# Kernel tuning notes

Measured on AMD Instinct MI355X. Metric: run time of the kernel, lower is better.

## Reference

```python
import jax, jax.numpy as jnp
import numpy as np

K_NB = 16
HID = 64
CIN = 128
EPS = 1e-5


def knn_idx(q, t, k):
    # q [B,N,3] queries, t [B,M,3] targets -> idx [B,N,k] into targets
    d = (jnp.sum(q * q, -1)[:, :, None] + jnp.sum(t * t, -1)[:, None, :]
         - 2.0 * jnp.einsum('bnd,bmd->bnm', q, t))
    _, idx = jax.lax.top_k(-d, k)
    return idx


def gather(feat, idx):
    # feat [B,C,M], idx [B,N,K] -> [B,C,N,K]
    return jax.vmap(lambda f, i: f[:, i])(feat, idx)


def conv1x1(x, W, b):
    # x [B,C,N,K], W [O,C], b [O]
    return jnp.einsum('oc,bcnk->bonk', W, x) + b[None, :, None, None]


def group_norm(x, gamma, beta, groups):
    B, C, N, K = x.shape
    xg = x.reshape(B, groups, C // groups, N, K)
    m = xg.mean(axis=(2, 3, 4), keepdims=True)
    v = xg.var(axis=(2, 3, 4), keepdims=True)
    xg = (xg - m) / jnp.sqrt(v + EPS)
    x = xg.reshape(B, C, N, K)
    return x * gamma[None, :, None, None] + beta[None, :, None, None]


def leaky(x):
    return jnp.where(x >= 0, x, 0.1 * x)


def setup_inputs() -> dict:
    key = jax.random.key(0)
    ks = jax.random.split(key, 20)
    B, N = 2, 4096
    d = {
        'xyz0': jax.random.normal(ks[0], (B, 3, N), jnp.float32),
        'xyz1': jax.random.normal(ks[1], (B, 3, N), jnp.float32),
        'state': jax.random.normal(ks[2], (B, HID, N), jnp.float32),
        'corr0': jax.random.normal(ks[3], (B, HID, N), jnp.float32),
        'feat0': jax.random.normal(ks[4], (B, CIN, N), jnp.float32),
        'feat1': jax.random.normal(ks[5], (B, CIN, N), jnp.float32),
        'flow0': jax.random.normal(ks[6], (B, 3, N), jnp.float32),
        # flow_layer: SetConv(3, [64,64]) -> convs take 3+3=6 then 64 in-chans
        'fw1': jax.random.normal(ks[7], (64, 6), jnp.float32) * 0.05,
        'fb1': jnp.zeros((64,), jnp.float32),
        'fg1': jnp.ones((64,), jnp.float32),
        'fbe1': jnp.zeros((64,), jnp.float32),
        'fw2': jax.random.normal(ks[8], (64, 64), jnp.float32) * 0.05,
        'fb2': jnp.zeros((64,), jnp.float32),
        'fg2': jnp.ones((64,), jnp.float32),
        'fbe2': jnp.zeros((64,), jnp.float32),
        # GRU gates: SetConv in_feat = hid(64)+(hid+64=128)=192, +3 = 195 -> 64, no act
        'wz': jax.random.normal(ks[9], (HID, 195), jnp.float32) * 0.05,
        'bz': jnp.zeros((HID,), jnp.float32),
        'wr': jax.random.normal(ks[10], (HID, 195), jnp.float32) * 0.05,
        'br': jnp.zeros((HID,), jnp.float32),
        'wq': jax.random.normal(ks[11], (HID, 195), jnp.float32) * 0.05,
        'bq': jnp.zeros((HID,), jnp.float32),
        # interp weight_net: 2*128+3=259 -> 128 -> 64
        'wa1': jax.random.normal(ks[12], (CIN, 2 * CIN + 3), jnp.float32) * 0.05,
        'ba1': jnp.zeros((CIN,), jnp.float32),
        'wa2': jax.random.normal(ks[13], (HID, CIN), jnp.float32) * 0.05,
        'ba2': jnp.zeros((HID,), jnp.float32),
    }
    return d


def reference(xyz0, xyz1, state, corr0, feat0, feat1, flow0,
              fw1, fb1, fg1, fbe1, fw2, fb2, fg2, fbe2,
              wz, bz, wr, br, wq, bq, wa1, ba1, wa2, ba2):
    xyz0_t = xyz0.transpose(0, 2, 1)  # [B,N,3]
    xyz1_t = xyz1.transpose(0, 2, 1)

    # ---- flow_layer: SetConv (KNN, N==npoint so new_xyz = xyz0) ----
    idx0 = knn_idx(xyz0_t, xyz0_t, K_NB)              # [B,N,K]
    gxyz0 = gather(xyz0, idx0) - xyz0[:, :, :, None]  # [B,3,N,K]
    h = jnp.concatenate([gather(flow0, idx0), gxyz0], axis=1)  # [B,6,N,K]
    h = leaky(group_norm(conv1x1(h, fw1, fb1), fg1, fbe1, 64 // 16))
    h = leaky(group_norm(conv1x1(h, fw2, fb2), fg2, fbe2, 64 // 16))
    flow_feat = h.max(axis=3)  # [B,64,N]

    # ---- iter_layer: SetGRU over xyz0 neighbors ----
    feat_g = jnp.concatenate([corr0, flow_feat], axis=1)  # [B,128,N]

    def gate(f, W, b):
        g = jnp.concatenate([gather(f, idx0), gxyz0], axis=1)
        return conv1x1(g, W, b).max(axis=3)  # [B,64,N]

    hid_in = jnp.concatenate([feat_g, state], axis=1)  # [B,192,N]
    z = jax.nn.sigmoid(gate(hid_in, wz, bz))
    r = jax.nn.sigmoid(gate(hid_in, wr, br))
    q = jnp.tanh(gate(jnp.concatenate([feat_g, r * state], axis=1), wq, bq))
    next_state = (1.0 - z) * state + z * q  # [B,64,N]

    # ---- align_layer: SetInterp (queries xyz1, targets xyz0) ----
    idx1 = knn_idx(xyz1_t, xyz0_t, K_NB)
    gv = gather(next_state, idx1)                        # [B,64,N,K]
    gx = gather(xyz0, idx1) - xyz1[:, :, :, None]        # [B,3,N,K]
    gf = jnp.concatenate([
        gather(feat0, idx1),
        jnp.broadcast_to(feat1[:, :, :, None], feat1.shape + (K_NB,))], axis=1)
    w = conv1x1(jnp.concatenate([gf, gx], axis=1), wa1, ba1)
    w = conv1x1(leaky(w), wa2, ba2)
    w = jax.nn.softmax(w, axis=3)
    return jnp.sum(gv * w, axis=3)  # [B,64,N]
```

## Files before the change

kernel.cpp:

```cpp
#include <hip/hip_runtime.h>

#define B_SZ 2

__device__ __forceinline__ int rfl(int x) { return __builtin_amdgcn_readfirstlane(x); }
__device__ __forceinline__ float leaky(float v) { return v >= 0.f ? v : 0.1f * v; }

__launch_bounds__(256)
__global__ void pack_kernel(const float* __restrict__ xyz, float4* __restrict__ out, int N)
{
  int b = blockIdx.y;
  int i = blockIdx.x * 256 + threadIdx.x;
  if (i >= N) return;
  const float* p = xyz + (size_t)b * 3 * N;
  float x = p[i], y = p[N + i], z = p[2 * N + i];
  out[(size_t)b * N + i] = make_float4(x, y, z, x * x + y * y + z * z);
}

__launch_bounds__(256)
__global__ void knn_wave_kernel(const float4* __restrict__ pk,
    const float* __restrict__ q0, const float* __restrict__ q1,
    int* __restrict__ idx0, int* __restrict__ idx1, int N, int PN)
{
  __shared__ __align__(16) float4 ts[1024];
  __shared__ uint2 buf[4][256];
  const int lane = threadIdx.x & 63, wav = rfl(threadIdx.x >> 6);
  const int qg = blockIdx.x * 4 + wav;
  const bool src1 = qg >= PN;
  const int qloc = src1 ? qg - PN : qg;
  const int b = qloc / N;
  const int n = qloc - b * N;
  const float* qb = (src1 ? q1 : q0) + (size_t)b * 3 * N;
  const float qx = qb[n], qy = qb[N + n], qz = qb[2 * N + n];
  const float qq = qx * qx + qy * qy + qz * qz;
  const float4* pb = pk + (size_t)b * N;

  float lmin = 3.0e38f;
  for (int ch = 0; ch < N; ch += 1024) {
    __syncthreads();
    for (int i = threadIdx.x; i < 1024; i += 256) ts[i] = pb[ch + i];
    __syncthreads();
#pragma unroll 4
    for (int sub = 0; sub < 16; ++sub) {
      float4 v = ts[sub * 64 + lane];
      float key = (qq + v.w) - 2.0f * (qx * v.x + qy * v.y + qz * v.z);
      lmin = fminf(lmin, key);
    }
  }
  float gm = fminf(lmin, __shfl_xor(lmin, 1, 64));
  gm = fminf(gm, __shfl_xor(gm, 2, 64));
  float t0 = gm;
  t0 = fmaxf(t0, __shfl_xor(t0, 4, 64));
  t0 = fmaxf(t0, __shfl_xor(t0, 8, 64));
  t0 = fmaxf(t0, __shfl_xor(t0, 16, 64));
  t0 = fmaxf(t0, __shfl_xor(t0, 32, 64));

  int cnt = 0;
  for (int ch = 0; ch < N; ch += 1024) {
    __syncthreads();
    for (int i = threadIdx.x; i < 1024; i += 256) ts[i] = pb[ch + i];
    __syncthreads();
    for (int sub = 0; sub < 16; ++sub) {
      float4 v = ts[sub * 64 + lane];
      float key = (qq + v.w) - 2.0f * (qx * v.x + qy * v.y + qz * v.z);
      bool qf = key <= t0;
      unsigned long long mask = __ballot(qf);
      if (mask) {
        unsigned lo = __builtin_amdgcn_mbcnt_lo((unsigned)mask, 0u);
        unsigned pre = __builtin_amdgcn_mbcnt_hi((unsigned)(mask >> 32), lo);
        if (qf) {
          unsigned slot = (unsigned)cnt + pre;
          if (slot < 256u)
            buf[wav][slot] = make_uint2(__float_as_uint(key),
                                        (unsigned)(ch + sub * 64 + lane));
        }
        cnt += (int)__popcll(mask);
      }
    }
  }
  int C = cnt < 256 ? cnt : 256;
  int* op = src1 ? idx1 : idx0;
  size_t base = ((size_t)b * N + n) * 16;

  if (C <= 64) {
    float kd = 3.0e38f; int ki = 0x7fffffff;
    if (lane < C) { uint2 u = buf[wav][lane]; kd = __uint_as_float(u.x); ki = (int)u.y; }
    int rank = 0;
    for (int j = 0; j < C; ++j) {
      uint2 u = buf[wav][j];
      float kj = __uint_as_float(u.x); int ij = (int)u.y;
      rank += ((kj < kd) || (kj == kd && ij < ki)) ? 1 : 0;
    }
    if (lane < C && rank < 16) op[base + rank] = ki;
  } else {
    float kd[4]; int ki[4]; int rank[4] = {0, 0, 0, 0};
#pragma unroll
    for (int e = 0; e < 4; ++e) {
      int j = e * 64 + lane;
      if (j < C) { uint2 u = buf[wav][j]; kd[e] = __uint_as_float(u.x); ki[e] = (int)u.y; }
      else { kd[e] = 3.0e38f; ki[e] = 0x7fffffff; }
    }
    for (int j = 0; j < C; ++j) {
      uint2 u = buf[wav][j];
      float kj = __uint_as_float(u.x); int ij = (int)u.y;
#pragma unroll
      for (int e = 0; e < 4; ++e)
        rank[e] += ((kj < kd[e]) || (kj == kd[e] && ij < ki[e])) ? 1 : 0;
    }
#pragma unroll
    for (int e = 0; e < 4; ++e)
      if (e * 64 + lane < C && rank[e] < 16) op[base + rank[e]] = ki[e];
  }
}

__launch_bounds__(256)
__global__ void prep_w_kernel(const float* __restrict__ wz, const float* __restrict__ wr,
    const float* __restrict__ wq, const float* __restrict__ wa1, const float* __restrict__ wa2,
    const float* __restrict__ bz, const float* __restrict__ br,
    float* __restrict__ WtZR, float* __restrict__ WtQ,
    float* __restrict__ WtU, float* __restrict__ WtV, float* __restrict__ WtA2,
    float* __restrict__ bZR)
{
  int job = blockIdx.x;
  int tid = threadIdx.x;
  if (job == 0) {
    for (int e = tid; e < 195 * 128; e += 256) {
      int k = e >> 7, o = e & 127;
      const float* w = (o < 64) ? wz : wr;
      WtZR[(size_t)k * 128 + o] = w[(size_t)(o & 63) * 195 + k];
    }
    if (tid < 128) bZR[tid] = (tid < 64) ? bz[tid] : br[tid - 64];
  } else if (job == 1) {
    for (int e = tid; e < 195 * 64; e += 256) {
      int k = e >> 6, o = e & 63;
      WtQ[(size_t)k * 64 + o] = wq[(size_t)o * 195 + k];
    }
  } else if (job == 2) {
    for (int e = tid; e < 131 * 128; e += 256) {
      int k = e >> 7, o = e & 127;
      int col = (k < 128) ? k : 256 + (k - 128);
      WtU[(size_t)k * 128 + o] = wa1[(size_t)o * 259 + col];
    }
  } else if (job == 3) {
    for (int e = tid; e < 131 * 128; e += 256) {
      int k = e >> 7, o = e & 127;
      float v = (k < 128) ? wa1[(size_t)o * 259 + 128 + k]
                          : -wa1[(size_t)o * 259 + 256 + (k - 128)];
      WtV[(size_t)k * 128 + o] = v;
    }
  } else {
    for (int e = tid; e < 128 * 64; e += 256) {
      int c = e >> 6, o = e & 63;
      WtA2[e] = wa2[(size_t)o * 128 + c];
    }
  }
}

#define KC 66
__launch_bounds__(256)
__global__ void projT_kernel(const float* __restrict__ Wt, int K, int WOUT,
    const float* __restrict__ bias, float* __restrict__ out,
    int N, int PN,
    const float* __restrict__ s0, int c0, int l0,
    const float* __restrict__ s1, int c1, int l1,
    const float* __restrict__ s2, int c2, int l2,
    const float* __restrict__ s3, int c3, int l3)
{
  __shared__ __align__(16) float Ws[KC][68];
  __shared__ __align__(16) float Xs[KC][68];
  const int n0 = blockIdx.x * 64;
  const int oo = blockIdx.y * 64;
  const int b = n0 / N;
  const int nn0 = n0 - b * N;
  const int tid = threadIdx.x;
  const int tx = tid & 15, ty = tid >> 4;
  const int o4 = tx * 4, n4 = ty * 4;
  float acc[4][4];
#pragma unroll
  for (int i = 0; i < 4; ++i)
#pragma unroll
    for (int j = 0; j < 4; ++j)
      acc[i][j] = bias ? bias[oo + o4 + j] : 0.0f;

  const int e01 = c0 + c1, e012 = c0 + c1 + c2;
  for (int k0 = 0; k0 < K; k0 += KC) {
    const int kc = min(KC, K - k0);
    __syncthreads();
    for (int e = tid; e < kc * 64; e += 256) {
      int k = e >> 6, o = e & 63;
      Ws[k][o] = Wt[(size_t)(k0 + k) * WOUT + oo + o];
    }
    for (int e = tid; e < kc * 64; e += 256) {
      int k = e >> 6, j = e & 63;
      int c = k0 + k;
      float v;
      if (c < c0)        v = l0 ? s0[(size_t)c * PN + n0 + j]
                                : s0[((size_t)b * c0 + c) * N + nn0 + j];
      else if (c < e01)  { int cc = c - c0;
                           v = l1 ? s1[(size_t)cc * PN + n0 + j]
                                  : s1[((size_t)b * c1 + cc) * N + nn0 + j]; }
      else if (c < e012) { int cc = c - e01;
                           v = l2 ? s2[(size_t)cc * PN + n0 + j]
                                  : s2[((size_t)b * c2 + cc) * N + nn0 + j]; }
      else               { int cc = c - e012;
                           v = l3 ? s3[(size_t)cc * PN + n0 + j]
                                  : s3[((size_t)b * c3 + cc) * N + nn0 + j]; }
      Xs[k][j] = v;
    }
    __syncthreads();
#pragma unroll 2
    for (int k = 0; k < kc; ++k) {
      float4 wv = *(const float4*)&Ws[k][o4];
      float4 xv = *(const float4*)&Xs[k][n4];
      acc[0][0] = fmaf(xv.x, wv.x, acc[0][0]); acc[0][1] = fmaf(xv.x, wv.y, acc[0][1]);
      acc[0][2] = fmaf(xv.x, wv.z, acc[0][2]); acc[0][3] = fmaf(xv.x, wv.w, acc[0][3]);
      acc[1][0] = fmaf(xv.y, wv.x, acc[1][0]); acc[1][1] = fmaf(xv.y, wv.y, acc[1][1]);
      acc[1][2] = fmaf(xv.y, wv.z, acc[1][2]); acc[1][3] = fmaf(xv.y, wv.w, acc[1][3]);
      acc[2][0] = fmaf(xv.z, wv.x, acc[2][0]); acc[2][1] = fmaf(xv.z, wv.y, acc[2][1]);
      acc[2][2] = fmaf(xv.z, wv.z, acc[2][2]); acc[2][3] = fmaf(xv.z, wv.w, acc[2][3]);
      acc[3][0] = fmaf(xv.w, wv.x, acc[3][0]); acc[3][1] = fmaf(xv.w, wv.y, acc[3][1]);
      acc[3][2] = fmaf(xv.w, wv.z, acc[3][2]); acc[3][3] = fmaf(xv.w, wv.w, acc[3][3]);
    }
  }
#pragma unroll
  for (int i = 0; i < 4; ++i) {
    float4 r = make_float4(acc[i][0], acc[i][1], acc[i][2], acc[i][3]);
    *(float4*)&out[(size_t)(n0 + n4 + i) * WOUT + oo + o4] = r;
  }
}

__launch_bounds__(256)
__global__ void projUV_kernel(const float* __restrict__ WtU, const float* __restrict__ WtV,
    const float* __restrict__ ba1, float* __restrict__ Uo, float* __restrict__ Vo,
    int N, int PN,
    const float* __restrict__ feat0, const float* __restrict__ feat1,
    const float* __restrict__ x0, const float* __restrict__ x1)
{
  __shared__ __align__(16) float Ws[KC][68];
  __shared__ __align__(16) float Xs[KC][68];
  const int z = blockIdx.z;
  const float* Wt = z ? WtV : WtU;
  const float* bias = z ? ba1 : 0;
  float* out = z ? Vo : Uo;
  const float* s0 = z ? feat1 : feat0;
  const float* s1 = z ? x1 : x0;
  const int K = 131, WOUT = 128, c0 = 128;
  const int n0 = blockIdx.x * 64;
  const int oo = blockIdx.y * 64;
  const int b = n0 / N;
  const int nn0 = n0 - b * N;
  const int tid = threadIdx.x;
  const int tx = tid & 15, ty = tid >> 4;
  const int o4 = tx * 4, n4 = ty * 4;
  float acc[4][4];
#pragma unroll
  for (int i = 0; i < 4; ++i)
#pragma unroll
    for (int j = 0; j < 4; ++j)
      acc[i][j] = bias ? bias[oo + o4 + j] : 0.0f;

  for (int k0 = 0; k0 < K; k0 += KC) {
    const int kc = min(KC, K - k0);
    __syncthreads();
    for (int e = tid; e < kc * 64; e += 256) {
      int k = e >> 6, o = e & 63;
      Ws[k][o] = Wt[(size_t)(k0 + k) * WOUT + oo + o];
    }
    for (int e = tid; e < kc * 64; e += 256) {
      int k = e >> 6, j = e & 63;
      int c = k0 + k;
      float v;
      if (c < c0) v = s0[((size_t)b * c0 + c) * N + nn0 + j];
      else        v = s1[((size_t)b * 3 + (c - c0)) * N + nn0 + j];
      Xs[k][j] = v;
    }
    __syncthreads();
#pragma unroll 2
    for (int k = 0; k < kc; ++k) {
      float4 wv = *(const float4*)&Ws[k][o4];
      float4 xv = *(const float4*)&Xs[k][n4];
      acc[0][0] = fmaf(xv.x, wv.x, acc[0][0]); acc[0][1] = fmaf(xv.x, wv.y, acc[0][1]);
      acc[0][2] = fmaf(xv.x, wv.z, acc[0][2]); acc[0][3] = fmaf(xv.x, wv.w, acc[0][3]);
      acc[1][0] = fmaf(xv.y, wv.x, acc[1][0]); acc[1][1] = fmaf(xv.y, wv.y, acc[1][1]);
      acc[1][2] = fmaf(xv.y, wv.z, acc[1][2]); acc[1][3] = fmaf(xv.y, wv.w, acc[1][3]);
      acc[2][0] = fmaf(xv.z, wv.x, acc[2][0]); acc[2][1] = fmaf(xv.z, wv.y, acc[2][1]);
      acc[2][2] = fmaf(xv.z, wv.z, acc[2][2]); acc[2][3] = fmaf(xv.z, wv.w, acc[2][3]);
      acc[3][0] = fmaf(xv.w, wv.x, acc[3][0]); acc[3][1] = fmaf(xv.w, wv.y, acc[3][1]);
      acc[3][2] = fmaf(xv.w, wv.z, acc[3][2]); acc[3][3] = fmaf(xv.w, wv.w, acc[3][3]);
    }
  }
#pragma unroll
  for (int i = 0; i < 4; ++i) {
    float4 r = make_float4(acc[i][0], acc[i][1], acc[i][2], acc[i][3]);
    *(float4*)&out[(size_t)(n0 + n4 + i) * WOUT + oo + o4] = r;
  }
}

__device__ __forceinline__ void seg_accumL(const float* __restrict__ p, int cnt,
    const float* __restrict__ WL, int sC, int sN, long n0, float acc[4])
{
#pragma unroll 4
  for (int c = 0; c < cnt; ++c) {
    float w = WL[c];
    const float* pp = p + (size_t)c * sC + (size_t)n0 * sN;
#pragma unroll
    for (int m = 0; m < 4; ++m)
      acc[m] = fmaf(w, pp[(size_t)m * sN], acc[m]);
  }
}

template<int WP>
__launch_bounds__(256)
__global__ void proj_kernel(
    const float* __restrict__ W0, const float* __restrict__ bias,
    float* __restrict__ out, int OUTS, int wld, int N,
    const float* __restrict__ s0, int c0, int w0,
    const float* __restrict__ s1, int c1, int w1)
{
  __shared__ float Wl[64 * WP];
  const int b = blockIdx.y;
  const int lane = threadIdx.x & 63;
  const int wav = rfl(threadIdx.x >> 6);
  for (int r = wav; r < 64; r += 4)
    for (int c = lane; c < c0; c += 64)
      Wl[r * WP + c] = W0[(size_t)r * wld + w0 + c];
  for (int r = wav; r < 64; r += 4)
    for (int c = lane; c < c1; c += 64)
      Wl[r * WP + c0 + c] = W0[(size_t)r * wld + w1 + c];
  __syncthreads();
  const long n0 = ((long)blockIdx.x * 4 + wav) * 4;
  float bv = bias ? bias[lane] : 0.0f;
  float acc[4] = {bv, bv, bv, bv};
  const float* WL = &Wl[lane * WP];
  seg_accumL(s0 + (size_t)b * c0 * N, c0, WL, N, 1, n0, acc);
  seg_accumL(s1 + (size_t)b * c1 * N, c1, WL + c0, N, 1, n0, acc);
#pragma unroll
  for (int m = 0; m < 4; ++m)
    out[((size_t)b * N + n0 + m) * OUTS + lane] = acc[m];
}

__launch_bounds__(256)
__global__ void gn1_stats_kernel(const float* __restrict__ G1, const float* __restrict__ xyz0,
    const float* __restrict__ fw1, const int* __restrict__ idx0,
    float* __restrict__ stats1, int N)
{
  __shared__ float red[4][4][2];
  int b = blockIdx.y;
  int lane = threadIdx.x & 63, wav = rfl(threadIdx.x >> 6);
  float wg0 = fw1[lane * 6 + 3], wg1 = fw1[lane * 6 + 4], wg2 = fw1[lane * 6 + 5];
  const float* xb = xyz0 + (size_t)b * 3 * N;
  float sum = 0.f, sq = 0.f;
  for (int n = blockIdx.x * 4 + wav; n < N; n += gridDim.x * 4) {
    const int* ip = idx0 + ((size_t)b * N + n) * 16;
    float bx = wg0 * xb[n] + wg1 * xb[N + n] + wg2 * xb[2 * N + n];
#pragma unroll
    for (int k = 0; k < 16; ++k) {
      int m = ip[k];
      float y = G1[((size_t)b * N + m) * 64 + lane] - bx;
      sum += y; sq += y * y;
    }
  }
#pragma unroll
  for (int off = 1; off < 16; off <<= 1) {
    sum += __shfl_xor(sum, off, 64);
    sq += __shfl_xor(sq, off, 64);
  }
  int g = lane >> 4;
  if ((lane & 15) == 0) { red[wav][g][0] = sum; red[wav][g][1] = sq; }
  __syncthreads();
  if (threadIdx.x < 8) {
    int gg = threadIdx.x >> 1, s = threadIdx.x & 1;
    float v = red[0][gg][s] + red[1][gg][s] + red[2][gg][s] + red[3][gg][s];
    atomicAdd(&stats1[(b * 4 + gg) * 2 + s], v);
  }
}

__launch_bounds__(256, 2)
__global__ void conv2_kernel(const float* __restrict__ G1, const float* __restrict__ xyz0,
    const float* __restrict__ fw1, const int* __restrict__ idx0,
    const float* __restrict__ fw2, const float* __restrict__ fb2,
    const float* __restrict__ fg1, const float* __restrict__ fbe1,
    const float* __restrict__ raw1, float cnt,
    float* __restrict__ y2max, float* __restrict__ y2min,
    float* __restrict__ stats2, int N)
{
  __shared__ __align__(16) float x2[4][16][64];
  __shared__ float red[4][4][2];
  const int b = blockIdx.y;
  const int lane = threadIdx.x & 63;
  const int wav = rfl(threadIdx.x >> 6);
  float4 w[16];
#pragma unroll
  for (int i = 0; i < 16; ++i) w[i] = *(const float4*)&fw2[lane * 64 + i * 4];
  float wg0 = fw1[lane * 6 + 3], wg1 = fw1[lane * 6 + 4], wg2 = fw1[lane * 6 + 5];
  const int g = lane >> 4;
  float s_ = raw1[(b * 4 + g) * 2], q_ = raw1[(b * 4 + g) * 2 + 1];
  float mu1 = s_ / cnt;
  float inv1 = rsqrtf(q_ / cnt - mu1 * mu1 + 1e-5f);
  float sc1 = fg1[lane] * inv1;
  float sh1 = fbe1[lane] - mu1 * sc1;
  float fb2l = fb2[lane];
  const float* xb = xyz0 + (size_t)b * 3 * N;
  float sum = 0.f, sq = 0.f;
  for (int n = blockIdx.x * 4 + wav; n < N; n += gridDim.x * 4) {
    const int* ip = idx0 + ((size_t)b * N + n) * 16;
    float bx = wg0 * xb[n] + wg1 * xb[N + n] + wg2 * xb[2 * N + n];
#pragma unroll
    for (int k = 0; k < 16; ++k) {
      int m = ip[k];
      float y = G1[((size_t)b * N + m) * 64 + lane] - bx;
      x2[wav][k][lane] = leaky(y * sc1 + sh1);
    }
    float acc[16];
#pragma unroll
    for (int k = 0; k < 16; ++k) acc[k] = fb2l;
#pragma unroll
    for (int c4 = 0; c4 < 16; ++c4) {
      float4 w4 = w[c4];
#pragma unroll
      for (int k = 0; k < 16; ++k) {
        float4 x4 = *(const float4*)&x2[wav][k][c4 * 4];
        acc[k] = fmaf(w4.x, x4.x, acc[k]);
        acc[k] = fmaf(w4.y, x4.y, acc[k]);
        acc[k] = fmaf(w4.z, x4.z, acc[k]);
        acc[k] = fmaf(w4.w, x4.w, acc[k]);
      }
    }
    float mx = -3.0e38f, mn = 3.0e38f;
#pragma unroll
    for (int k = 0; k < 16; ++k) {
      mx = fmaxf(mx, acc[k]); mn = fminf(mn, acc[k]);
      sum += acc[k]; sq += acc[k] * acc[k];
    }
    y2max[((size_t)b * N + n) * 64 + lane] = mx;
    y2min[((size_t)b * N + n) * 64 + lane] = mn;
  }
#pragma unroll
  for (int off = 1; off < 16; off <<= 1) {
    sum += __shfl_xor(sum, off, 64);
    sq += __shfl_xor(sq, off, 64);
  }
  if ((lane & 15) == 0) { red[wav][g][0] = sum; red[wav][g][1] = sq; }
  __syncthreads();
  if (threadIdx.x < 8) {
    int gg = threadIdx.x >> 1, s = threadIdx.x & 1;
    float v = red[0][gg][s] + red[1][gg][s] + red[2][gg][s] + red[3][gg][s];
    atomicAdd(&stats2[(b * 4 + gg) * 2 + s], v);
  }
}

__launch_bounds__(256)
__global__ void flow_feat_kernel(const float* __restrict__ y2max, const float* __restrict__ y2min,
    const float* __restrict__ raw2, float cnt,
    const float* __restrict__ fg2, const float* __restrict__ fbe2,
    float* __restrict__ ff_t, int N, int PN)
{
  size_t i = (size_t)blockIdx.x * blockDim.x + threadIdx.x;
  if (i >= (size_t)B_SZ * N * 64) return;
  int c = i & 63;
  size_t pn = i >> 6;
  int b = (int)(pn / N);
  int g = c >> 4;
  float s_ = raw2[(b * 4 + g) * 2], q_ = raw2[(b * 4 + g) * 2 + 1];
  float mu = s_ / cnt;
  float inv = rsqrtf(q_ / cnt - mu * mu + 1e-5f);
  float sc = fg2[c] * inv;
  float sh = fbe2[c] - mu * sc;
  float y = (sc >= 0.0f) ? y2max[i] : y2min[i];
  ff_t[(size_t)c * PN + pn] = leaky(y * sc + sh);
}

__launch_bounds__(256)
__global__ void gate_zr_kernel(const float* __restrict__ Szr,
    const float* __restrict__ wz, const float* __restrict__ wr,
    const float* __restrict__ xyz0, const float* __restrict__ state,
    const int* __restrict__ idx0,
    float* __restrict__ zo, float* __restrict__ rs_t, int N, int PN)
{
  int b = blockIdx.y;
  int lane = threadIdx.x & 63, wav = rfl(threadIdx.x >> 6);
  float wz0 = wz[lane * 195 + 192], wz1 = wz[lane * 195 + 193], wz2 = wz[lane * 195 + 194];
  float wr0 = wr[lane * 195 + 192], wr1 = wr[lane * 195 + 193], wr2 = wr[lane * 195 + 194];
  const float* xb = xyz0 + (size_t)b * 3 * N;
  for (int n = blockIdx.x * 4 + wav; n < N; n += gridDim.x * 4) {
    const int* ip = idx0 + ((size_t)b * N + n) * 16;
    float u0 = xb[n], u1 = xb[N + n], u2 = xb[2 * N + n];
    float xz = wz0 * u0 + wz1 * u1 + wz2 * u2;
    float xr = wr0 * u0 + wr1 * u1 + wr2 * u2;
    float mz = -3.0e38f, mr = -3.0e38f;
#pragma unroll
    for (int k = 0; k < 16; ++k) {
      size_t mo = ((size_t)b * N + ip[k]) * 128 + lane;
      mz = fmaxf(mz, Szr[mo]);
      mr = fmaxf(mr, Szr[mo + 64]);
    }
    size_t no = ((size_t)b * N + n) * 64 + lane;
    float z = 1.f / (1.f + expf(-(mz - xz)));
    float r = 1.f / (1.f + expf(-(mr - xr)));
    zo[no] = z;
    rs_t[(size_t)lane * PN + (size_t)b * N + n] = r * state[((size_t)b * 64 + lane) * N + n];
  }
}

__launch_bounds__(256)
__global__ void gate_q_ns_kernel(const float* __restrict__ Sq, const float* __restrict__ wq,
    const float* __restrict__ xyz0, const float* __restrict__ zo,
    const float* __restrict__ state, const int* __restrict__ idx0,
    float* __restrict__ ns, int N)
{
  int b = blockIdx.y;
  int lane = threadIdx.x & 63, wav = rfl(threadIdx.x >> 6);
  float wq0 = wq[lane * 195 + 192], wq1 = wq[lane * 195 + 193], wq2 = wq[lane * 195 + 194];
  const float* xb = xyz0 + (size_t)b * 3 * N;
  for (int n = blockIdx.x * 4 + wav; n < N; n += gridDim.x * 4) {
    const int* ip = idx0 + ((size_t)b * N + n) * 16;
    float xq = wq0 * xb[n] + wq1 * xb[N + n] + wq2 * xb[2 * N + n];
    float mq = -3.0e38f;
#pragma unroll
    for (int k = 0; k < 16; ++k)
      mq = fmaxf(mq, Sq[((size_t)b * N + ip[k]) * 64 + lane]);
    size_t no = ((size_t)b * N + n) * 64 + lane;
    float q = tanhf(mq - xq);
    float z = zo[no];
    float st = state[((size_t)b * 64 + lane) * N + n];
    ns[no] = (1.f - z) * st + z * q;
  }
}

__launch_bounds__(256, 2)
__global__ void align_kernel(const float* __restrict__ U, const float* __restrict__ V,
    const float* __restrict__ WtA2, const float* __restrict__ ba2,
    const float* __restrict__ ns, const int* __restrict__ idx1,
    float* __restrict__ out, int N)
{
  __shared__ __align__(16) float Xs[64][128];
  __shared__ __align__(16) float Ws[128][64];
  const int b = blockIdx.y;
  const int tid = threadIdx.x;
  const int lane = tid & 63;
  const int wav = rfl(tid >> 6);

  for (int e = tid; e < 2048; e += 256) {
    int c = e >> 4, o4 = (e & 15) << 2;
    *(float4*)&Ws[c][o4] = *(const float4*)&WtA2[(c << 6) + o4];
  }

  const int n = blockIdx.x * 4 + wav;
  int mkreg = 0;
  {
    const int* ip = idx1 + ((size_t)b * N + n) * 16;
    if (lane < 16) mkreg = ip[lane];
  }
  const int c4l = lane & 31;
  const int half = lane >> 5;
  float4 v4 = *(const float4*)&V[(((size_t)b * N + n) << 7) + (c4l << 2)];
  for (int k0 = 0; k0 < 16; k0 += 2) {
    int k = k0 + half;
    int m = __shfl(mkreg, k);
    float4 u4 = *(const float4*)&U[(((size_t)b * N + m) << 7) + (c4l << 2)];
    float4 xv;
    xv.x = leaky(u4.x + v4.x);
    xv.y = leaky(u4.y + v4.y);
    xv.z = leaky(u4.z + v4.z);
    xv.w = leaky(u4.w + v4.w);
    int row = (wav << 4) + k;
    *(float4*)&Xs[row][(c4l ^ (row & 7)) << 2] = xv;
  }
  __syncthreads();

  const int tx = tid & 15, ty = tid >> 4;
  const int o4 = tx << 2, r0 = ty << 2;
  float4 bav = *(const float4*)&ba2[o4];
  float acc[4][4];
#pragma unroll
  for (int i = 0; i < 4; ++i) {
    acc[i][0] = bav.x; acc[i][1] = bav.y; acc[i][2] = bav.z; acc[i][3] = bav.w;
  }
  for (int c4 = 0; c4 < 32; ++c4) {
    float4 wv0 = *(const float4*)&Ws[c4 * 4 + 0][o4];
    float4 wv1 = *(const float4*)&Ws[c4 * 4 + 1][o4];
    float4 wv2 = *(const float4*)&Ws[c4 * 4 + 2][o4];
    float4 wv3 = *(const float4*)&Ws[c4 * 4 + 3][o4];
#pragma unroll
    for (int i = 0; i < 4; ++i) {
      int row = r0 + i;
      float4 xv = *(const float4*)&Xs[row][(c4 ^ (row & 7)) << 2];
      acc[i][0] = fmaf(xv.x, wv0.x, acc[i][0]);
      acc[i][1] = fmaf(xv.x, wv0.y, acc[i][1]);
      acc[i][2] = fmaf(xv.x, wv0.z, acc[i][2]);
      acc[i][3] = fmaf(xv.x, wv0.w, acc[i][3]);
      acc[i][0] = fmaf(xv.y, wv1.x, acc[i][0]);
      acc[i][1] = fmaf(xv.y, wv1.y, acc[i][1]);
      acc[i][2] = fmaf(xv.y, wv1.z, acc[i][2]);
      acc[i][3] = fmaf(xv.y, wv1.w, acc[i][3]);
      acc[i][0] = fmaf(xv.z, wv2.x, acc[i][0]);
      acc[i][1] = fmaf(xv.z, wv2.y, acc[i][1]);
      acc[i][2] = fmaf(xv.z, wv2.z, acc[i][2]);
      acc[i][3] = fmaf(xv.z, wv2.w, acc[i][3]);
      acc[i][0] = fmaf(xv.w, wv3.x, acc[i][0]);
      acc[i][1] = fmaf(xv.w, wv3.y, acc[i][1]);
      acc[i][2] = fmaf(xv.w, wv3.z, acc[i][2]);
      acc[i][3] = fmaf(xv.w, wv3.w, acc[i][3]);
    }
  }

  float m_[4];
#pragma unroll
  for (int j = 0; j < 4; ++j) {
    float m = fmaxf(fmaxf(acc[0][j], acc[1][j]), fmaxf(acc[2][j], acc[3][j]));
    m = fmaxf(m, __shfl_xor(m, 16, 64));
    m = fmaxf(m, __shfl_xor(m, 32, 64));
    m_[j] = m;
  }
  float e_[4][4], s_[4];
#pragma unroll
  for (int j = 0; j < 4; ++j) {
    float s = 0.f;
#pragma unroll
    for (int i = 0; i < 4; ++i) { e_[i][j] = expf(acc[i][j] - m_[j]); s += e_[i][j]; }
    s += __shfl_xor(s, 16, 64);
    s += __shfl_xor(s, 32, 64);
    s_[j] = s;
  }
  float o_[4] = {0.f, 0.f, 0.f, 0.f};
#pragma unroll
  for (int i = 0; i < 4; ++i) {
    int k = (r0 + i) & 15;
    int m = __shfl(mkreg, k);
    float4 nsv = *(const float4*)&ns[(((size_t)b * N + m) << 6) + o4];
    o_[0] = fmaf(e_[i][0], nsv.x, o_[0]);
    o_[1] = fmaf(e_[i][1], nsv.y, o_[1]);
    o_[2] = fmaf(e_[i][2], nsv.z, o_[2]);
    o_[3] = fmaf(e_[i][3], nsv.w, o_[3]);
  }
#pragma unroll
  for (int j = 0; j < 4; ++j) {
    o_[j] += __shfl_xor(o_[j], 16, 64);
    o_[j] += __shfl_xor(o_[j], 32, 64);
  }
  if ((lane >> 4) == 0) {
#pragma unroll
    for (int j = 0; j < 4; ++j)
      out[((size_t)b * 64 + o4 + j) * N + n] = o_[j] / s_[j];
  }
}

extern "C" void kernel_launch(void* const* d_in, const int* in_sizes, int n_in,
                              void* d_out, int out_size, void* d_ws, size_t ws_size,
                              hipStream_t stream) {
  (void)n_in; (void)out_size; (void)ws_size;
  const float* xyz0 = (const float*)d_in[0];
  const float* xyz1 = (const float*)d_in[1];
  const float* state = (const float*)d_in[2];
  const float* corr0 = (const float*)d_in[3];
  const float* feat0 = (const float*)d_in[4];
  const float* feat1 = (const float*)d_in[5];
  const float* flow0 = (const float*)d_in[6];
  const float* fw1 = (const float*)d_in[7];
  const float* fb1 = (const float*)d_in[8];
  const float* fg1 = (const float*)d_in[9];
  const float* fbe1 = (const float*)d_in[10];
  const float* fw2 = (const float*)d_in[11];
  const float* fb2 = (const float*)d_in[12];
  const float* fg2 = (const float*)d_in[13];
  const float* fbe2 = (const float*)d_in[14];
  const float* wz = (const float*)d_in[15];
  const float* bz = (const float*)d_in[16];
  const float* wr = (const float*)d_in[17];
  const float* br = (const float*)d_in[18];
  const float* wq = (const float*)d_in[19];
  const float* bq = (const float*)d_in[20];
  const float* wa1 = (const float*)d_in[21];
  const float* ba1 = (const float*)d_in[22];
  const float* wa2 = (const float*)d_in[23];
  const float* ba2 = (const float*)d_in[24];
  float* out = (float*)d_out;

  const int N = in_sizes[0] / (3 * B_SZ);
  const int PN = B_SZ * N;
  char* wsb = (char*)d_ws;
  size_t off = 0;
  auto take = [&](size_t bytes) -> char* {
    char* p = wsb + off;
    off += (bytes + 255) & ~(size_t)255;
    return p;
  };
  float* U    = (float*)take((size_t)PN * 128 * 4);
  float* V    = (float*)take((size_t)PN * 128 * 4);
  float* Szr  = (float*)take((size_t)PN * 128 * 4);
  float4* pk0 = (float4*)take((size_t)PN * 4 * 4);
  int*   idx0 = (int*)  take((size_t)PN * 16 * 4);
  int*   idx1 = (int*)  take((size_t)PN * 16 * 4);
  float* G1   = (float*)take((size_t)PN * 64 * 4);
  float* y2mx = (float*)take((size_t)PN * 64 * 4);
  float* y2mn = (float*)take((size_t)PN * 64 * 4);
  float* ff_t = (float*)take((size_t)PN * 64 * 4);
  float* Sq   = (float*)take((size_t)PN * 64 * 4);
  float* zg   = (float*)take((size_t)PN * 64 * 4);
  float* rs_t = (float*)take((size_t)PN * 64 * 4);
  float* ns   = (float*)take((size_t)PN * 64 * 4);
  float* WtZR = (float*)take(195 * 128 * 4);
  float* WtQ  = (float*)take(195 * 64 * 4);
  float* WtU  = (float*)take(131 * 128 * 4);
  float* WtV  = (float*)take(131 * 128 * 4);
  float* WtA2 = (float*)take(128 * 64 * 4);
  float* bZR  = (float*)take(128 * 4);
  float* stats = (float*)take(256);
  float* raw1 = stats, *raw2 = stats + 16;

  const float cntv = 16.0f * N * 16.0f;

  hipMemsetAsync(raw1, 0, 32 * sizeof(float), stream);

  pack_kernel<<<dim3((N + 255) / 256, B_SZ), 256, 0, stream>>>(xyz0, pk0, N);
  prep_w_kernel<<<5, 256, 0, stream>>>(wz, wr, wq, wa1, wa2, bz, br,
      WtZR, WtQ, WtU, WtV, WtA2, bZR);
  knn_wave_kernel<<<dim3(2 * PN / 4), 256, 0, stream>>>(pk0, xyz0, xyz1, idx0, idx1, N, PN);

  proj_kernel<7><<<dim3(N / 16, B_SZ), 256, 0, stream>>>(
      fw1, fb1, G1, 64, 6, N, flow0, 3, 0, xyz0, 3, 3);

  gn1_stats_kernel<<<dim3(256, B_SZ), 256, 0, stream>>>(G1, xyz0, fw1, idx0, raw1, N);
  conv2_kernel<<<dim3(512, B_SZ), 256, 0, stream>>>(G1, xyz0, fw1, idx0, fw2, fb2, fg1, fbe1,
      raw1, cntv, y2mx, y2mn, raw2, N);
  flow_feat_kernel<<<dim3((unsigned)((size_t)PN * 64 / 256)), 256, 0, stream>>>(
      y2mx, y2mn, raw2, cntv, fg2, fbe2, ff_t, N, PN);

  projT_kernel<<<dim3(PN / 64, 2), 256, 0, stream>>>(WtZR, 195, 128, bZR, Szr, N, PN,
      corr0, 64, 0,  ff_t, 64, 1,  state, 64, 0,  xyz0, 3, 0);

  gate_zr_kernel<<<dim3(256, B_SZ), 256, 0, stream>>>(Szr, wz, wr, xyz0, state, idx0, zg, rs_t, N, PN);

  projT_kernel<<<dim3(PN / 64, 1), 256, 0, stream>>>(WtQ, 195, 64, bq, Sq, N, PN,
      corr0, 64, 0,  ff_t, 64, 1,  rs_t, 64, 1,  xyz0, 3, 0);

  gate_q_ns_kernel<<<dim3(256, B_SZ), 256, 0, stream>>>(Sq, wq, xyz0, zg, state, idx0, ns, N);

  projUV_kernel<<<dim3(PN / 64, 2, 2), 256, 0, stream>>>(WtU, WtV, ba1, U, V, N, PN,
      feat0, feat1, xyz0, xyz1);

  align_kernel<<<dim3(N / 4, B_SZ), 256, 0, stream>>>(U, V, WtA2, ba2, ns, idx1, out, N);
}
```

Measured before the change: 349.1 us.

## Split KNN into per-thread threshold pass and wave-per-query select pass

The threshold pass of the KNN kernel moves into a separate kernel where each thread handles one query. It takes the max of 16 per-segment minima over the contiguous target segments, using uniform broadcast loads instead of a wave-per-query LDS scan. The select kernel reads this threshold, pads it slightly for rounding, and keeps the ballot-based candidate collection. Candidate capacity grows to 320 to cover the new bound. This removes one full LDS sweep per query from the select kernel, at the cost of an extra launch, a small global buffer, and possible overflow if candidates exceed capacity.

Result: slower. 376.6 us (+7.9%).

```diff
diff --git a/kernel.cpp b/kernel.cpp
--- a/kernel.cpp
+++ b/kernel.cpp
@@ -1,6 +1,7 @@
 #include <hip/hip_runtime.h>
 
 #define B_SZ 2
+#define CAP 320
 
 __device__ __forceinline__ int rfl(int x) { return __builtin_amdgcn_readfirstlane(x); }
 __device__ __forceinline__ float leaky(float v) { return v >= 0.f ? v : 0.1f * v; }
@@ -17,12 +18,52 @@
 }
 
 __launch_bounds__(256)
-__global__ void knn_wave_kernel(const float4* __restrict__ pk,
+__global__ void knn_thresh_kernel(const float4* __restrict__ pk,
     const float* __restrict__ q0, const float* __restrict__ q1,
+    float* __restrict__ t0arr, int N, int PN)
+{
+  __shared__ float bounds[4][64];
+  const int lane = threadIdx.x & 63;
+  const int wav = rfl(threadIdx.x >> 6);
+  const int qg = blockIdx.x * 64 + lane;
+  const bool src1 = qg >= PN;
+  const int qloc = src1 ? qg - PN : qg;
+  const int b = qloc / N;
+  const int n = qloc - b * N;
+  const float* qb = (src1 ? q1 : q0) + (size_t)b * 3 * N;
+  const float qx = qb[n], qy = qb[N + n], qz = qb[2 * N + n];
+  const float qq = qx * qx + qy * qy + qz * qz;
+  const int SEG = N >> 4;
+  const float4* pb = pk + (size_t)b * N + (size_t)wav * (N >> 2);
+
+  float m0 = 3.0e38f, m1 = 3.0e38f, m2 = 3.0e38f, m3 = 3.0e38f;
+  for (int i = 0; i < SEG; ++i) {
+    float4 v0 = pb[i];
+    float4 v1 = pb[SEG + i];
+    float4 v2 = pb[2 * SEG + i];
+    float4 v3 = pb[3 * SEG + i];
+    m0 = fminf(m0, (qq + v0.w) - 2.0f * (qx * v0.x + qy * v0.y + qz * v0.z));
+    m1 = fminf(m1, (qq + v1.w) - 2.0f * (qx * v1.x + qy * v1.y + qz * v1.z));
+    m2 = fminf(m2, (qq + v2.w) - 2.0f * (qx * v2.x + qy * v2.y + qz * v2.z));
+    m3 = fminf(m3, (qq + v3.w) - 2.0f * (qx * v3.x + qy * v3.y + qz * v3.z));
+  }
+  bounds[wav][lane] = fmaxf(fmaxf(m0, m1), fmaxf(m2, m3));
+  __syncthreads();
+  if (wav == 0) {
+    float t0 = fmaxf(fmaxf(bounds[0][lane], bounds[1][lane]),
+                     fmaxf(bounds[2][lane], bounds[3][lane]));
+    t0arr[qg] = t0;
+  }
+}
+
+__launch_bounds__(256)
+__global__ void knn_select_kernel(const float4* __restrict__ pk,
+    const float* __restrict__ q0, const float* __restrict__ q1,
+    const float* __restrict__ t0arr,
     int* __restrict__ idx0, int* __restrict__ idx1, int N, int PN)
 {
   __shared__ __align__(16) float4 ts[1024];
-  __shared__ uint2 buf[4][256];
+  __shared__ uint2 buf[4][CAP];
   const int lane = threadIdx.x & 63, wav = rfl(threadIdx.x >> 6);
   const int qg = blockIdx.x * 4 + wav;
   const bool src1 = qg >= PN;
@@ -32,27 +73,9 @@
   const float* qb = (src1 ? q1 : q0) + (size_t)b * 3 * N;
   const float qx = qb[n], qy = qb[N + n], qz = qb[2 * N + n];
   const float qq = qx * qx + qy * qy + qz * qz;
+  float t0 = t0arr[qg];
+  t0 += fabsf(t0) * 1e-4f + 1e-12f;
   const float4* pb = pk + (size_t)b * N;
-
-  float lmin = 3.0e38f;
-  for (int ch = 0; ch < N; ch += 1024) {
-    __syncthreads();
-    for (int i = threadIdx.x; i < 1024; i += 256) ts[i] = pb[ch + i];
-    __syncthreads();
-#pragma unroll 4
-    for (int sub = 0; sub < 16; ++sub) {
-      float4 v = ts[sub * 64 + lane];
-      float key = (qq + v.w) - 2.0f * (qx * v.x + qy * v.y + qz * v.z);
-      lmin = fminf(lmin, key);
-    }
-  }
-  float gm = fminf(lmin, __shfl_xor(lmin, 1, 64));
-  gm = fminf(gm, __shfl_xor(gm, 2, 64));
-  float t0 = gm;
-  t0 = fmaxf(t0, __shfl_xor(t0, 4, 64));
-  t0 = fmaxf(t0, __shfl_xor(t0, 8, 64));
-  t0 = fmaxf(t0, __shfl_xor(t0, 16, 64));
-  t0 = fmaxf(t0, __shfl_xor(t0, 32, 64));
 
   int cnt = 0;
   for (int ch = 0; ch < N; ch += 1024) {
@@ -69,7 +92,7 @@
         unsigned pre = __builtin_amdgcn_mbcnt_hi((unsigned)(mask >> 32), lo);
         if (qf) {
           unsigned slot = (unsigned)cnt + pre;
-          if (slot < 256u)
+          if (slot < (unsigned)CAP)
             buf[wav][slot] = make_uint2(__float_as_uint(key),
                                         (unsigned)(ch + sub * 64 + lane));
         }
@@ -77,7 +100,7 @@
       }
     }
   }
-  int C = cnt < 256 ? cnt : 256;
+  int C = cnt < CAP ? cnt : CAP;
   int* op = src1 ? idx1 : idx0;
   size_t base = ((size_t)b * N + n) * 16;
 
@@ -92,9 +115,9 @@
     }
     if (lane < C && rank < 16) op[base + rank] = ki;
   } else {
-    float kd[4]; int ki[4]; int rank[4] = {0, 0, 0, 0};
-#pragma unroll
-    for (int e = 0; e < 4; ++e) {
+    float kd[5]; int ki[5]; int rank[5] = {0, 0, 0, 0, 0};
+#pragma unroll
+    for (int e = 0; e < 5; ++e) {
       int j = e * 64 + lane;
       if (j < C) { uint2 u = buf[wav][j]; kd[e] = __uint_as_float(u.x); ki[e] = (int)u.y; }
       else { kd[e] = 3.0e38f; ki[e] = 0x7fffffff; }
@@ -103,11 +126,11 @@
       uint2 u = buf[wav][j];
       float kj = __uint_as_float(u.x); int ij = (int)u.y;
 #pragma unroll
-      for (int e = 0; e < 4; ++e)
+      for (int e = 0; e < 5; ++e)
         rank[e] += ((kj < kd[e]) || (kj == kd[e] && ij < ki[e])) ? 1 : 0;
     }
 #pragma unroll
-    for (int e = 0; e < 4; ++e)
+    for (int e = 0; e < 5; ++e)
       if (e * 64 + lane < C && rank[e] < 16) op[base + rank[e]] = ki[e];
   }
 }
@@ -690,6 +713,7 @@
   float4* pk0 = (float4*)take((size_t)PN * 4 * 4);
   int*   idx0 = (int*)  take((size_t)PN * 16 * 4);
   int*   idx1 = (int*)  take((size_t)PN * 16 * 4);
+  float* t0a  = (float*)take((size_t)2 * PN * 4);
   float* G1   = (float*)take((size_t)PN * 64 * 4);
   float* y2mx = (float*)take((size_t)PN * 64 * 4);
   float* y2mn = (float*)take((size_t)PN * 64 * 4);
@@ -714,7 +738,9 @@
   pack_kernel<<<dim3((N + 255) / 256, B_SZ), 256, 0, stream>>>(xyz0, pk0, N);
   prep_w_kernel<<<5, 256, 0, stream>>>(wz, wr, wq, wa1, wa2, bz, br,
       WtZR, WtQ, WtU, WtV, WtA2, bZR);
-  knn_wave_kernel<<<dim3(2 * PN / 4), 256, 0, stream>>>(pk0, xyz0, xyz1, idx0, idx1, N, PN);
+  knn_thresh_kernel<<<dim3(2 * PN / 64), 256, 0, stream>>>(pk0, xyz0, xyz1, t0a, N, PN);
+  knn_select_kernel<<<dim3(2 * PN / 4), 256, 0, stream>>>(pk0, xyz0, xyz1, t0a,
+      idx0, idx1, N, PN);
 
   proj_kernel<7><<<dim3(N / 16, B_SZ), 256, 0, stream>>>(
       fw1, fb1, G1, 64, 6, N, flow0, 3, 0, xyz0, 3, 3);
```
